# Kernel optimization log

Hardware: AMD Instinct MI355X
Metric: run time of the kernel (lower is better)

Reference implementation:

```python
import jax, jax.numpy as jnp
import numpy as np

N = 50000       # nodes
E = 800000      # edges (avg degree 16)
IN_DIM = 128
EDGE_DIM = 32
OUT_DIM = 128


def setup_inputs() -> dict:
    key = jax.random.key(0)
    ks = jax.random.split(key, 7)
    nfeat = jax.random.normal(ks[0], (N, IN_DIM), jnp.float32)
    etype = jax.random.normal(ks[1], (E, EDGE_DIM), jnp.float32)
    src = jax.random.randint(ks[2], (E,), 0, N)
    dst = jax.random.randint(ks[3], (E,), 0, N)
    scaled = lambda k, shape, fan: jax.random.normal(k, shape, jnp.float32) / np.sqrt(fan).astype(np.float32)
    W_edge = scaled(ks[4], (OUT_DIM, EDGE_DIM), EDGE_DIM)          # edge_map.weight
    W_ne = scaled(ks[5], (OUT_DIM, IN_DIM + OUT_DIM), IN_DIM + OUT_DIM)  # fc_neigh_edge.weight
    b_ne = jnp.zeros((OUT_DIM,), jnp.float32)
    W_self = scaled(ks[6], (OUT_DIM, IN_DIM), IN_DIM)              # fc_self.weight
    b_self = jnp.zeros((OUT_DIM,), jnp.float32)
    eps = jnp.zeros((1,), jnp.float32)                             # init_eps = 0, not learned
    return dict(nfeat=nfeat, etype=etype, src=src, dst=dst,
                W_edge=W_edge, W_ne=W_ne, b_ne=b_ne,
                W_self=W_self, b_self=b_self, eps=eps)


def reference(nfeat, etype, src, dst, W_edge, W_ne, b_ne, W_self, b_self, eps):
    # per-edge message: relu(fc_neigh_edge(cat(src_h, edge_map(etype))))
    # split W_ne to avoid materializing the concatenated [E, in+out] tensor
    W1 = W_ne[:, :IN_DIM]    # acts on src node features
    W2 = W_ne[:, IN_DIM:]    # acts on mapped edge features
    eh = etype @ W_edge.T                              # [E, out]
    src_h = nfeat[src]                                 # gather [E, in]
    m = jax.nn.relu(src_h @ W1.T + eh @ W2.T + b_ne)   # [E, out]
    # max-reduce messages to destination nodes (DGL max reducer; 0 for isolated nodes)
    neigh = jax.ops.segment_max(m, dst, num_segments=N)
    deg = jax.ops.segment_sum(jnp.ones((E,), m.dtype), dst, num_segments=N)
    neigh = jnp.where((deg > 0)[:, None], neigh, jnp.zeros((), m.dtype))
    out = (1.0 + eps) * neigh + (nfeat @ W_self.T + b_self)
    return out
```

## Files before the change

### kernel.cpp

```cpp
#include <hip/hip_runtime.h>
#include <hip/hip_bf16.h>

#define NNODES 50000
#define NEDGES 800000
#define IN_DIM 128
#define EDGE_DIM 32
#define OUT_DIM 128
#define KDIM 160
#define A_STRIDE 168
#define NS 136
#define MT_STRIDE 72
#define NT (NEDGES / 64)
#define EG 1024
#define NSCB 49

typedef __attribute__((ext_vector_type(8))) short short8;
typedef __attribute__((ext_vector_type(4))) short short4v;
typedef __attribute__((ext_vector_type(4))) float floatx4;

__device__ __forceinline__ short f2bf(float f) {
    union { float f; unsigned u; } v; v.f = f;
    unsigned r = (v.u + 0x7FFFu + ((v.u >> 16) & 1u)) >> 16;
    return (short)r;
}

__device__ __forceinline__ void store_bf4(short* p, floatx4 v) {
    short4v s;
    s.x = f2bf(v.x); s.y = f2bf(v.y); s.z = f2bf(v.z); s.w = f2bf(v.w);
    *(short4v*)p = s;
}

__device__ __forceinline__ void store_bf8(short* p, floatx4 a, floatx4 b) {
    short8 s;
    s[0] = f2bf(a.x); s[1] = f2bf(a.y); s[2] = f2bf(a.z); s[3] = f2bf(a.w);
    s[4] = f2bf(b.x); s[5] = f2bf(b.y); s[6] = f2bf(b.z); s[7] = f2bf(b.w);
    *(short8*)p = s;
}

#define MFMA8(ACC, A0, A1, B0, B1, B2, B3)                                        \
    ACC[0][0] = __builtin_amdgcn_mfma_f32_16x16x32_bf16(A0, B0, ACC[0][0], 0, 0, 0); \
    ACC[0][1] = __builtin_amdgcn_mfma_f32_16x16x32_bf16(A0, B1, ACC[0][1], 0, 0, 0); \
    ACC[0][2] = __builtin_amdgcn_mfma_f32_16x16x32_bf16(A0, B2, ACC[0][2], 0, 0, 0); \
    ACC[0][3] = __builtin_amdgcn_mfma_f32_16x16x32_bf16(A0, B3, ACC[0][3], 0, 0, 0); \
    ACC[1][0] = __builtin_amdgcn_mfma_f32_16x16x32_bf16(A1, B0, ACC[1][0], 0, 0, 0); \
    ACC[1][1] = __builtin_amdgcn_mfma_f32_16x16x32_bf16(A1, B1, ACC[1][1], 0, 0, 0); \
    ACC[1][2] = __builtin_amdgcn_mfma_f32_16x16x32_bf16(A1, B2, ACC[1][2], 0, 0, 0); \
    ACC[1][3] = __builtin_amdgcn_mfma_f32_16x16x32_bf16(A1, B3, ACC[1][3], 0, 0, 0);

__global__ __launch_bounds__(256) void prep_kernel(
    const float* __restrict__ nfeat, const int* __restrict__ dst,
    const float* __restrict__ W_edge, const float* __restrict__ W_ne,
    const float* __restrict__ W_self,
    int* __restrict__ cnt, short* __restrict__ nfB,
    short* __restrict__ WcatB, short* __restrict__ WselfB)
{
    int gid = blockIdx.x * 256 + threadIdx.x;
    int GS = gridDim.x * 256;
    for (int i = gid; i < NNODES * IN_DIM / 8; i += GS) {
        floatx4 a = ((const floatx4*)nfeat)[2 * i];
        floatx4 b = ((const floatx4*)nfeat)[2 * i + 1];
        store_bf8(nfB + 8 * i, a, b);
    }
    for (int idx = gid; idx < OUT_DIM * KDIM + OUT_DIM * IN_DIM; idx += GS) {
        if (idx < OUT_DIM * KDIM) {
            int n = idx / KDIM, k = idx - n * KDIM;
            float val;
            if (k < IN_DIM) {
                val = W_ne[n * 256 + k];
            } else {
                int j = k - IN_DIM;
                float s = 0.f;
                for (int kk = 0; kk < 128; ++kk)
                    s += W_ne[n * 256 + 128 + kk] * W_edge[kk * 32 + j];
                val = s;
            }
            WcatB[idx] = f2bf(val);
        } else {
            int s = idx - OUT_DIM * KDIM;
            WselfB[s] = f2bf(W_self[s]);
        }
    }
    for (int e = gid; e < NEDGES; e += GS)
        atomicAdd(&cnt[dst[e]], 1);
}

__global__ __launch_bounds__(256) void scan_part(const int* __restrict__ cnt,
                                                 int* __restrict__ bsum) {
    __shared__ int red[256];
    int b = blockIdx.x, t = threadIdx.x;
    int idx = b * 1024 + t * 4;
    int4 v = {0, 0, 0, 0};
    if (idx < NNODES) v = *(const int4*)(cnt + idx);
    red[t] = v.x + v.y + v.z + v.w;
    __syncthreads();
    for (int off = 128; off > 0; off >>= 1) {
        if (t < off) red[t] += red[t + off];
        __syncthreads();
    }
    if (t == 0) bsum[b] = red[0];
}

__global__ __launch_bounds__(64) void scan_mid(const int* __restrict__ bsum,
                                               int* __restrict__ boff) {
    __shared__ int a[64], b[64];
    int t = threadIdx.x;
    int v = (t < NSCB) ? bsum[t] : 0;
    a[t] = v;
    __syncthreads();
    int* in = a; int* out = b;
    for (int off = 1; off < 64; off <<= 1) {
        out[t] = in[t] + (t >= off ? in[t - off] : 0);
        __syncthreads();
        int* tmp = in; in = out; out = tmp;
    }
    if (t < NSCB) boff[t] = in[t] - v;
}

__global__ __launch_bounds__(256) void scan_write(const int* __restrict__ cnt,
                                                  const int* __restrict__ boff,
                                                  int* __restrict__ cur) {
    __shared__ int a[256], bb[256];
    int b = blockIdx.x, t = threadIdx.x;
    int idx = b * 1024 + t * 4;
    int4 v = {0, 0, 0, 0};
    if (idx < NNODES) v = *(const int4*)(cnt + idx);
    int s = v.x + v.y + v.z + v.w;
    a[t] = s;
    __syncthreads();
    int* in = a; int* out = bb;
    for (int off = 1; off < 256; off <<= 1) {
        out[t] = in[t] + (t >= off ? in[t - off] : 0);
        __syncthreads();
        int* tmp = in; in = out; out = tmp;
    }
    if (idx < NNODES) {
        int base = boff[b] + in[t] - s;
        cur[idx] = base;     base += v.x;
        cur[idx + 1] = base; base += v.y;
        cur[idx + 2] = base; base += v.z;
        cur[idx + 3] = base;
    }
}

__global__ __launch_bounds__(256) void scatter_kernel(
    const int* __restrict__ src, const int* __restrict__ dst,
    const float* __restrict__ etype,
    int* __restrict__ cur,
    int* __restrict__ esd, short* __restrict__ escT) {
    const int tid = threadIdx.x;
    const int lane = tid & 63;
    const int g = lane & 7;
    const int ldr = lane & ~7;
    const int grp = tid >> 3;
    const int GS = gridDim.x * 32;
    for (int e = blockIdx.x * 32 + grp; e < NEDGES; e += GS) {
        int pos = 0;
        if (g == 0) {
            int d = dst[e];
            int s = src[e];
            pos = atomicAdd(&cur[d], 1);
            esd[pos] = (int)((unsigned)s | ((unsigned)d << 16));
        }
        pos = __shfl(pos, ldr);
        floatx4 v = ((const floatx4*)(etype + (size_t)e * 32))[g];
        store_bf4(escT + (size_t)pos * 32 + g * 4, v);
    }
}

__global__ __launch_bounds__(256, 4) void edge_kernel(
    const short* __restrict__ nfB, const short* __restrict__ escT,
    const int* __restrict__ esd, const float* __restrict__ b_ne,
    const short* __restrict__ WcatB, float* __restrict__ out)
{
    __shared__ short As[64 * A_STRIDE];
    __shared__ unsigned short mT[128 * MT_STRIDE];
    __shared__ short dstL[2][64];

    const int tid = threadIdx.x;
    const int lane = tid & 63;
    const int w = tid >> 6;
    const int li = lane & 15, q = lane >> 4;

    short8 bf[2][5];
    #pragma unroll
    for (int ct = 0; ct < 2; ++ct)
        #pragma unroll
        for (int kk = 0; kk < 5; ++kk)
            bf[ct][kk] = *(const short8*)(WcatB +
                (size_t)(w * 32 + ct * 16 + li) * KDIM + kk * 32 + q * 8);

    float bias[2];
    #pragma unroll
    for (int ct = 0; ct < 2; ++ct) bias[ct] = b_ne[w * 32 + ct * 16 + li];

    const int ee = tid >> 2, ec = tid & 3;

    short8 pv0, pv1, pv2, pv3;
    short8 pe;
    int rsd = 0;
    int psd = 0;

    const int tA = blockIdx.x;

    {
        int sd = esd[tA * 64 + ee];
        int s = sd & 0xFFFF;
        const short8* nr = (const short8*)(nfB + (size_t)s * 128);
        pv0 = nr[4 * ec]; pv1 = nr[4 * ec + 1];
        pv2 = nr[4 * ec + 2]; pv3 = nr[4 * ec + 3];
        pe = *(const short8*)(escT + (size_t)(tA * 64 + ee) * 32 + ec * 8);

        int tB = tA + EG;
        int sdB = 0;
        if (tB < NT) sdB = esd[tB * 64 + ee];

        short* ap = As + ee * A_STRIDE + 32 * ec;
        *(short8*)(ap)      = pv0;
        *(short8*)(ap + 8)  = pv1;
        *(short8*)(ap + 16) = pv2;
        *(short8*)(ap + 24) = pv3;
        *(short8*)(As + ee * A_STRIDE + IN_DIM + 8 * ec) = pe;
        if (ec == 0) dstL[0][ee] = (short)((unsigned)sd >> 16);

        if (tB < NT) {
            int sB = sdB & 0xFFFF;
            const short8* nrB = (const short8*)(nfB + (size_t)sB * 128);
            pv0 = nrB[4 * ec]; pv1 = nrB[4 * ec + 1];
            pv2 = nrB[4 * ec + 2]; pv3 = nrB[4 * ec + 3];
            pe = *(const short8*)(escT + (size_t)(tB * 64 + ee) * 32 + ec * 8);
            rsd = sdB;
            int tC = tB + EG;
            if (tC < NT) psd = esd[tC * 64 + ee];
        }
    }

    int it = 0;
    for (int t = tA; t < NT; t += EG, ++it) {
        const int cb = it & 1, nb = cb ^ 1;

        asm volatile("s_waitcnt lgkmcnt(0)" ::: "memory");
        __builtin_amdgcn_s_barrier();

        floatx4 acc[4][2];
        #pragma unroll
        for (int i = 0; i < 4; ++i)
            #pragma unroll
            for (int j = 0; j < 2; ++j)
                acc[i][j] = (floatx4){0.f, 0.f, 0.f, 0.f};

        __builtin_amdgcn_s_setprio(1);
        #pragma unroll
        for (int kk = 0; kk < 5; ++kk) {
            short8 a0 = *(const short8*)(As + (0 * 16 + li) * A_STRIDE + kk * 32 + q * 8);
            short8 a1 = *(const short8*)(As + (1 * 16 + li) * A_STRIDE + kk * 32 + q * 8);
            short8 a2 = *(const short8*)(As + (2 * 16 + li) * A_STRIDE + kk * 32 + q * 8);
            short8 a3 = *(const short8*)(As + (3 * 16 + li) * A_STRIDE + kk * 32 + q * 8);
            acc[0][0] = __builtin_amdgcn_mfma_f32_16x16x32_bf16(a0, bf[0][kk], acc[0][0], 0, 0, 0);
            acc[0][1] = __builtin_amdgcn_mfma_f32_16x16x32_bf16(a0, bf[1][kk], acc[0][1], 0, 0, 0);
            acc[1][0] = __builtin_amdgcn_mfma_f32_16x16x32_bf16(a1, bf[0][kk], acc[1][0], 0, 0, 0);
            acc[1][1] = __builtin_amdgcn_mfma_f32_16x16x32_bf16(a1, bf[1][kk], acc[1][1], 0, 0, 0);
            acc[2][0] = __builtin_amdgcn_mfma_f32_16x16x32_bf16(a2, bf[0][kk], acc[2][0], 0, 0, 0);
            acc[2][1] = __builtin_amdgcn_mfma_f32_16x16x32_bf16(a2, bf[1][kk], acc[2][1], 0, 0, 0);
            acc[3][0] = __builtin_amdgcn_mfma_f32_16x16x32_bf16(a3, bf[0][kk], acc[3][0], 0, 0, 0);
            acc[3][1] = __builtin_amdgcn_mfma_f32_16x16x32_bf16(a3, bf[1][kk], acc[3][1], 0, 0, 0);
        }
        __builtin_amdgcn_s_setprio(0);

        #pragma unroll
        for (int rt = 0; rt < 4; ++rt) {
            #pragma unroll
            for (int ct = 0; ct < 2; ++ct) {
                floatx4 a = acc[rt][ct];
                short4v s;
                float v0 = a.x + bias[ct]; s.x = f2bf(v0 > 0.f ? v0 : 0.f);
                float v1 = a.y + bias[ct]; s.y = f2bf(v1 > 0.f ? v1 : 0.f);
                float v2 = a.z + bias[ct]; s.z = f2bf(v2 > 0.f ? v2 : 0.f);
                float v3 = a.w + bias[ct]; s.w = f2bf(v3 > 0.f ? v3 : 0.f);
                *(short4v*)((short*)mT + (w * 32 + ct * 16 + li) * MT_STRIDE
                            + rt * 16 + q * 4) = s;
            }
        }
        asm volatile("s_waitcnt lgkmcnt(0)" ::: "memory");
        __builtin_amdgcn_s_barrier();

        {
            int tn = t + EG;
            if (tn < NT) {
                short* ap = As + ee * A_STRIDE + 32 * ec;
                *(short8*)(ap)      = pv0;
                *(short8*)(ap + 8)  = pv1;
                *(short8*)(ap + 16) = pv2;
                *(short8*)(ap + 24) = pv3;
                *(short8*)(As + ee * A_STRIDE + IN_DIM + 8 * ec) = pe;
                if (ec == 0) dstL[nb][ee] = (short)((unsigned)rsd >> 16);

                int sd2 = psd;
                int t2 = tn + EG;
                if (t2 < NT) {
                    int t3 = t2 + EG;
                    if (t3 < NT) psd = esd[t3 * 64 + ee];
                    int s2 = sd2 & 0xFFFF;
                    const short8* nr2 = (const short8*)(nfB + (size_t)s2 * 128);
                    pv0 = nr2[4 * ec]; pv1 = nr2[4 * ec + 1];
                    pv2 = nr2[4 * ec + 2]; pv3 = nr2[4 * ec + 3];
                    pe = *(const short8*)(escT + (size_t)(t2 * 64 + ee) * 32 + ec * 8);
                    rsd = sd2;
                }
            }
        }
        __builtin_amdgcn_sched_barrier(0);

        {
            int c = tid & 127, h = tid >> 7;
            int r0 = h * 32;
            unsigned mval[32];
            #pragma unroll
            for (int j = 0; j < 4; ++j) {
                short8 v = *(const short8*)((const short*)mT + c * MT_STRIDE
                                            + r0 + 8 * j);
                #pragma unroll
                for (int k = 0; k < 8; ++k)
                    mval[8 * j + k] = (unsigned short)v[k];
            }
            const short8* dls = (const short8*)(&dstL[cb][r0]);
            int curd = 0;
            unsigned best = 0;
            #pragma unroll
            for (int j = 0; j < 4; ++j) {
                short8 dv = dls[j];
                #pragma unroll
                for (int k = 0; k < 8; ++k) {
                    int r = 8 * j + k;
                    int d = __builtin_amdgcn_readfirstlane(
                        (int)(unsigned short)dv[k]);
                    if (r == 0) {
                        curd = d; best = mval[0];
                    } else if (d != curd) {
                        atomicMax((int*)out + (size_t)curd * 128 + c,
                                  (int)(best << 16));
                        curd = d; best = mval[r];
                    } else {
                        best = best > mval[r] ? best : mval[r];
                    }
                }
            }
            atomicMax((int*)out + (size_t)curd * 128 + c, (int)(best << 16));
        }
    }
}

__global__ __launch_bounds__(256) void node_kernel(
    const short* __restrict__ nfB, const float* __restrict__ b_self,
    const float* __restrict__ eps, const short* __restrict__ WselfB,
    float* __restrict__ out)
{
    __shared__ short As[64 * NS];
    __shared__ short Bs[128 * NS];
    const int tid = threadIdx.x;
    const int n0 = blockIdx.x * 64;

    {
        int r = tid >> 1, h = tid & 1;
        const short8* g = (const short8*)(WselfB + r * 128 + h * 64);
        short* l = Bs + r * NS + h * 64;
        #pragma unroll
        for (int c = 0; c < 8; ++c)
            *(short8*)(l + 8 * c) = g[c];
    }
    {
        int r = tid >> 2, c = tid & 3;
        int n = n0 + r;
        short* ap = As + r * NS + 32 * c;
        if (n < NNODES) {
            const short8* nr = (const short8*)(nfB + (size_t)n * 128);
            #pragma unroll
            for (int j = 0; j < 4; ++j)
                *(short8*)(ap + 8 * j) = nr[4 * c + j];
        } else {
            #pragma unroll
            for (int j = 0; j < 4; ++j)
                *(short8*)(ap + 8 * j) = (short8){0,0,0,0,0,0,0,0};
        }
    }
    __syncthreads();

    const int lane = tid & 63;
    const int w = tid >> 6;
    const int et = w & 1;
    const int nh = w >> 1;
    const int li = lane & 15, q = lane >> 4;

    floatx4 acc[2][4];
    #pragma unroll
    for (int i = 0; i < 2; ++i)
        #pragma unroll
        for (int j = 0; j < 4; ++j)
            acc[i][j] = (floatx4){0.f, 0.f, 0.f, 0.f};

    const short* Ab = As + (et * 32 + li) * NS + q * 8;
    const short* Bb = Bs + (nh * 64 + li) * NS + q * 8;
    #pragma unroll
    for (int kk = 0; kk < 4; ++kk) {
        short8 a0 = *(const short8*)(Ab + kk * 32);
        short8 a1 = *(const short8*)(Ab + 16 * NS + kk * 32);
        short8 b0 = *(const short8*)(Bb + kk * 32);
        short8 b1 = *(const short8*)(Bb + 16 * NS + kk * 32);
        short8 b2 = *(const short8*)(Bb + 32 * NS + kk * 32);
        short8 b3 = *(const short8*)(Bb + 48 * NS + kk * 32);
        MFMA8(acc, a0, a1, b0, b1, b2, b3)
    }

    const float epsv = 1.0f + eps[0];
    #pragma unroll
    for (int ta = 0; ta < 2; ++ta) {
        #pragma unroll
        for (int r = 0; r < 4; ++r) {
            int n = n0 + et * 32 + ta * 16 + q * 4 + r;
            if (n < NNODES) {
                #pragma unroll
                for (int tb = 0; tb < 4; ++tb) {
                    int o = nh * 64 + tb * 16 + li;
                    float v = acc[ta][tb][r] + b_self[o]
                            + epsv * out[(size_t)n * 128 + o];
                    out[(size_t)n * 128 + o] = v;
                }
            }
        }
    }
}

__global__ void prep_w(const float* __restrict__ W_edge,
                       const float* __restrict__ W_ne,
                       const float* __restrict__ W_self,
                       short* __restrict__ WcatB, short* __restrict__ WselfB)
{
    int idx = blockIdx.x * 256 + threadIdx.x;
    if (idx < OUT_DIM * KDIM) {
        int n = idx / KDIM, k = idx - n * KDIM;
        float val;
        if (k < IN_DIM) {
            val = W_ne[n * 256 + k];
        } else {
            int j = k - IN_DIM;
            float s = 0.f;
            for (int kk = 0; kk < 128; ++kk)
                s += W_ne[n * 256 + 128 + kk] * W_edge[kk * 32 + j];
            val = s;
        }
        WcatB[idx] = f2bf(val);
    } else if (idx < OUT_DIM * KDIM + OUT_DIM * IN_DIM) {
        int s = idx - OUT_DIM * KDIM;
        WselfB[s] = f2bf(W_self[s]);
    }
}

__global__ __launch_bounds__(256) void edge_direct(
    const float* __restrict__ nfeat, const float* __restrict__ etype,
    const int* __restrict__ src, const int* __restrict__ dst,
    const float* __restrict__ b_ne, const short* __restrict__ WcatB,
    float* __restrict__ out)
{
    __shared__ short As[64 * A_STRIDE];
    __shared__ short Bs[128 * A_STRIDE];
    const int tid = threadIdx.x;
    const int e0 = blockIdx.x * 64;
    {
        int r = tid >> 1, h = tid & 1;
        const short8* g = (const short8*)(WcatB + r * KDIM + h * 80);
        short* l = Bs + r * A_STRIDE + h * 80;
        #pragma unroll
        for (int c = 0; c < 10; ++c) *(short8*)(l + 8 * c) = g[c];
    }
    {
        const floatx4* ge = (const floatx4*)(etype + (size_t)e0 * 32);
        #pragma unroll
        for (int i = 0; i < 2; ++i) {
            int f = tid + i * 256;
            int e = f >> 3, c = f & 7;
            store_bf4(As + e * A_STRIDE + IN_DIM + 4 * c, ge[f]);
        }
    }
    {
        int g = tid & 15, eo = tid >> 4;
        #pragma unroll
        for (int p = 0; p < 4; ++p) {
            int e = eo + p * 16;
            int s = src[e0 + e];
            const floatx4* row = (const floatx4*)(nfeat + (size_t)s * 128);
            floatx4 v0 = row[g];
            floatx4 v1 = row[g + 16];
            store_bf4(As + e * A_STRIDE + 4 * g, v0);
            store_bf4(As + e * A_STRIDE + 64 + 4 * g, v1);
        }
    }
    __syncthreads();
    const int lane = tid & 63;
    const int w = tid >> 6;
    const int et = w & 1, nh = w >> 1;
    const int li = lane & 15, q = lane >> 4;
    floatx4 acc[2][4];
    #pragma unroll
    for (int i = 0; i < 2; ++i)
        #pragma unroll
        for (int j = 0; j < 4; ++j)
            acc[i][j] = (floatx4){0.f, 0.f, 0.f, 0.f};
    const short* Ab = As + (et * 32 + li) * A_STRIDE + q * 8;
    const short* Bb = Bs + (nh * 64 + li) * A_STRIDE + q * 8;
    #pragma unroll
    for (int kk = 0; kk < 5; ++kk) {
        short8 a0 = *(const short8*)(Ab + kk * 32);
        short8 a1 = *(const short8*)(Ab + 16 * A_STRIDE + kk * 32);
        short8 b0 = *(const short8*)(Bb + kk * 32);
        short8 b1 = *(const short8*)(Bb + 16 * A_STRIDE + kk * 32);
        short8 b2 = *(const short8*)(Bb + 32 * A_STRIDE + kk * 32);
        short8 b3 = *(const short8*)(Bb + 48 * A_STRIDE + kk * 32);
        MFMA8(acc, a0, a1, b0, b1, b2, b3)
    }
    #pragma unroll
    for (int ta = 0; ta < 2; ++ta) {
        #pragma unroll
        for (int r = 0; r < 4; ++r) {
            int el = et * 32 + ta * 16 + q * 4 + r;
            int d = dst[e0 + el];
            int* nrow = (int*)out + (size_t)d * 128;
            #pragma unroll
            for (int tb = 0; tb < 4; ++tb) {
                int o = nh * 64 + tb * 16 + li;
                float v = acc[ta][tb][r] + b_ne[o];
                v = v > 0.f ? v : 0.f;
                atomicMax(nrow + o, __float_as_int(v));
            }
        }
    }
}

__global__ __launch_bounds__(256) void node_direct(
    const float* __restrict__ nfeat, const float* __restrict__ b_self,
    const float* __restrict__ eps, const short* __restrict__ WselfB,
    float* __restrict__ out)
{
    __shared__ short As[64 * NS];
    __shared__ short Bs[128 * NS];
    const int tid = threadIdx.x;
    const int n0 = blockIdx.x * 64;
    {
        int r = tid >> 1, h = tid & 1;
        const short8* g = (const short8*)(WselfB + r * 128 + h * 64);
        short* l = Bs + r * NS + h * 64;
        #pragma unroll
        for (int c = 0; c < 8; ++c) *(short8*)(l + 8 * c) = g[c];
    }
    {
        int r = tid >> 2, fi = tid & 3;
        int n = n0 + r;
        if (n < NNODES) {
            const floatx4* row = (const floatx4*)(nfeat + (size_t)n * 128);
            #pragma unroll
            for (int p = 0; p < 8; ++p) {
                int f = fi + 4 * p;
                store_bf4(As + r * NS + 4 * f, row[f]);
            }
        } else {
            #pragma unroll
            for (int p = 0; p < 8; ++p) {
                int f = fi + 4 * p;
                *(short4v*)(As + r * NS + 4 * f) = (short4v){0, 0, 0, 0};
            }
        }
    }
    __syncthreads();
    const int lane = tid & 63;
    const int w = tid >> 6;
    const int et = w & 1, nh = w >> 1;
    const int li = lane & 15, q = lane >> 4;
    floatx4 acc[2][4];
    #pragma unroll
    for (int i = 0; i < 2; ++i)
        #pragma unroll
        for (int j = 0; j < 4; ++j)
            acc[i][j] = (floatx4){0.f, 0.f, 0.f, 0.f};
    const short* Ab = As + (et * 32 + li) * NS + q * 8;
    const short* Bb = Bs + (nh * 64 + li) * NS + q * 8;
    #pragma unroll
    for (int kk = 0; kk < 4; ++kk) {
        short8 a0 = *(const short8*)(Ab + kk * 32);
        short8 a1 = *(const short8*)(Ab + 16 * NS + kk * 32);
        short8 b0 = *(const short8*)(Bb + kk * 32);
        short8 b1 = *(const short8*)(Bb + 16 * NS + kk * 32);
        short8 b2 = *(const short8*)(Bb + 32 * NS + kk * 32);
        short8 b3 = *(const short8*)(Bb + 48 * NS + kk * 32);
        MFMA8(acc, a0, a1, b0, b1, b2, b3)
    }
    const float epsv = 1.0f + eps[0];
    #pragma unroll
    for (int ta = 0; ta < 2; ++ta) {
        #pragma unroll
        for (int r = 0; r < 4; ++r) {
            int n = n0 + et * 32 + ta * 16 + q * 4 + r;
            if (n < NNODES) {
                #pragma unroll
                for (int tb = 0; tb < 4; ++tb) {
                    int o = nh * 64 + tb * 16 + li;
                    float v = acc[ta][tb][r] + b_self[o]
                            + epsv * out[(size_t)n * 128 + o];
                    out[(size_t)n * 128 + o] = v;
                }
            }
        }
    }
}

extern "C" void kernel_launch(void* const* d_in, const int* in_sizes, int n_in,
                              void* d_out, int out_size, void* d_ws, size_t ws_size,
                              hipStream_t stream) {
    const float* nfeat  = (const float*)d_in[0];
    const float* etype  = (const float*)d_in[1];
    const int*   src    = (const int*)d_in[2];
    const int*   dst    = (const int*)d_in[3];
    const float* W_edge = (const float*)d_in[4];
    const float* W_ne   = (const float*)d_in[5];
    const float* b_ne   = (const float*)d_in[6];
    const float* W_self = (const float*)d_in[7];
    const float* b_self = (const float*)d_in[8];
    const float* eps    = (const float*)d_in[9];
    float* out = (float*)d_out;

    char* ws = (char*)d_ws;
    size_t off = 0;
    auto alloc = [&](size_t bytes) { void* p = ws + off; off = (off + bytes + 255) & ~(size_t)255; return p; };
    int*   cnt    = (int*)alloc((size_t)NNODES * 4);
    int*   cur    = (int*)alloc((size_t)NNODES * 4);
    int*   esd    = (int*)alloc((size_t)NEDGES * 4);
    short* escT   = (short*)alloc((size_t)NEDGES * EDGE_DIM * 2);
    short* nfB    = (short*)alloc((size_t)NNODES * IN_DIM * 2);
    short* WcatB  = (short*)alloc((size_t)OUT_DIM * KDIM * 2);
    short* WselfB = (short*)alloc((size_t)OUT_DIM * IN_DIM * 2);
    int*   bsum   = (int*)alloc((size_t)NSCB * 4);
    int*   boff   = (int*)alloc((size_t)NSCB * 4);
    size_t need = off;

    if (ws_size >= need) {
        hipMemsetAsync(cnt, 0, (size_t)NNODES * 4, stream);
        hipMemsetAsync(out, 0, (size_t)NNODES * OUT_DIM * sizeof(float), stream);
        prep_kernel<<<1024, 256, 0, stream>>>(nfeat, dst, W_edge, W_ne, W_self,
                                              cnt, nfB, WcatB, WselfB);
        scan_part<<<NSCB, 256, 0, stream>>>(cnt, bsum);
        scan_mid<<<1, 64, 0, stream>>>(bsum, boff);
        scan_write<<<NSCB, 256, 0, stream>>>(cnt, boff, cur);
        scatter_kernel<<<2048, 256, 0, stream>>>(src, dst, etype, cur, esd, escT);
        edge_kernel<<<EG, 256, 0, stream>>>(nfB, escT, esd, b_ne, WcatB, out);
        node_kernel<<<(NNODES + 63) / 64, 256, 0, stream>>>(nfB, b_self, eps,
                                                            WselfB, out);
    } else {
        short* WcatB2  = (short*)d_ws;
        short* WselfB2 = WcatB2 + (size_t)OUT_DIM * KDIM;
        hipMemsetAsync(out, 0, (size_t)NNODES * 128 * sizeof(float), stream);
        prep_w<<<144, 256, 0, stream>>>(W_edge, W_ne, W_self, WcatB2, WselfB2);
        edge_direct<<<NEDGES / 64, 256, 0, stream>>>(nfeat, etype, src, dst,
                                                     b_ne, WcatB2, out);
        node_direct<<<(NNODES + 63) / 64, 256, 0, stream>>>(nfeat, b_self, eps,
                                                            WselfB2, out);
    }
}
```

Before: 345.9 us.

## Split edge scatter into index-only scatter and sorted-order etype gather

The combined scatter kernel, which atomically placed each edge and wrote its bf16 edge features to a scattered position, is replaced by two kernels. The first uses one thread per edge to do the atomic placement and records the original edge id alongside the packed src/dst. The second walks the sorted positions, gathers etype rows by original id and writes escT contiguously. The aim is coalesced writes and denser atomics, at the cost of an extra launch, an 8-byte epack array, and the edge kernel reading 8-byte records to get the 4-byte src/dst field.

```diff
diff --git a/kernel.cpp b/kernel.cpp
--- a/kernel.cpp
+++ b/kernel.cpp
@@ -142,34 +142,40 @@
     }
 }
 
-__global__ __launch_bounds__(256) void scatter_kernel(
-    const int* __restrict__ src, const int* __restrict__ dst,
-    const float* __restrict__ etype,
-    int* __restrict__ cur,
-    int* __restrict__ esd, short* __restrict__ escT) {
+__global__ void scatter_lite(const int* __restrict__ src,
+                             const int* __restrict__ dst,
+                             int* __restrict__ cur,
+                             int2* __restrict__ epack) {
+    int e = blockIdx.x * 256 + threadIdx.x;
+    if (e < NEDGES) {
+        int d = dst[e];
+        int s = src[e];
+        int pos = atomicAdd(&cur[d], 1);
+        int2 r;
+        r.x = (int)((unsigned)s | ((unsigned)d << 16));
+        r.y = e;
+        epack[pos] = r;
+    }
+}
+
+__global__ __launch_bounds__(256) void gather_conv(
+    const int2* __restrict__ epack, const float* __restrict__ etype,
+    short* __restrict__ escT) {
     const int tid = threadIdx.x;
     const int lane = tid & 63;
     const int g = lane & 7;
-    const int ldr = lane & ~7;
     const int grp = tid >> 3;
     const int GS = gridDim.x * 32;
-    for (int e = blockIdx.x * 32 + grp; e < NEDGES; e += GS) {
-        int pos = 0;
-        if (g == 0) {
-            int d = dst[e];
-            int s = src[e];
-            pos = atomicAdd(&cur[d], 1);
-            esd[pos] = (int)((unsigned)s | ((unsigned)d << 16));
-        }
-        pos = __shfl(pos, ldr);
+    for (int p = blockIdx.x * 32 + grp; p < NEDGES; p += GS) {
+        int e = epack[p].y;
         floatx4 v = ((const floatx4*)(etype + (size_t)e * 32))[g];
-        store_bf4(escT + (size_t)pos * 32 + g * 4, v);
+        store_bf4(escT + (size_t)p * 32 + g * 4, v);
     }
 }
 
 __global__ __launch_bounds__(256, 4) void edge_kernel(
     const short* __restrict__ nfB, const short* __restrict__ escT,
-    const int* __restrict__ esd, const float* __restrict__ b_ne,
+    const int2* __restrict__ epack, const float* __restrict__ b_ne,
     const short* __restrict__ WcatB, float* __restrict__ out)
 {
     __shared__ short As[64 * A_STRIDE];
@@ -203,7 +209,7 @@
     const int tA = blockIdx.x;
 
     {
-        int sd = esd[tA * 64 + ee];
+        int sd = epack[tA * 64 + ee].x;
         int s = sd & 0xFFFF;
         const short8* nr = (const short8*)(nfB + (size_t)s * 128);
         pv0 = nr[4 * ec]; pv1 = nr[4 * ec + 1];
@@ -212,7 +218,7 @@
 
         int tB = tA + EG;
         int sdB = 0;
-        if (tB < NT) sdB = esd[tB * 64 + ee];
+        if (tB < NT) sdB = epack[tB * 64 + ee].x;
 
         short* ap = As + ee * A_STRIDE + 32 * ec;
         *(short8*)(ap)      = pv0;
@@ -230,7 +236,7 @@
             pe = *(const short8*)(escT + (size_t)(tB * 64 + ee) * 32 + ec * 8);
             rsd = sdB;
             int tC = tB + EG;
-            if (tC < NT) psd = esd[tC * 64 + ee];
+            if (tC < NT) psd = epack[tC * 64 + ee].x;
         }
     }
 
@@ -298,7 +304,7 @@
                 int t2 = tn + EG;
                 if (t2 < NT) {
                     int t3 = t2 + EG;
-                    if (t3 < NT) psd = esd[t3 * 64 + ee];
+                    if (t3 < NT) psd = epack[t3 * 64 + ee].x;
                     int s2 = sd2 & 0xFFFF;
                     const short8* nr2 = (const short8*)(nfB + (size_t)s2 * 128);
                     pv0 = nr2[4 * ec]; pv1 = nr2[4 * ec + 1];
@@ -630,7 +636,7 @@
     auto alloc = [&](size_t bytes) { void* p = ws + off; off = (off + bytes + 255) & ~(size_t)255; return p; };
     int*   cnt    = (int*)alloc((size_t)NNODES * 4);
     int*   cur    = (int*)alloc((size_t)NNODES * 4);
-    int*   esd    = (int*)alloc((size_t)NEDGES * 4);
+    int2*  epack  = (int2*)alloc((size_t)NEDGES * 8);
     short* escT   = (short*)alloc((size_t)NEDGES * EDGE_DIM * 2);
     short* nfB    = (short*)alloc((size_t)NNODES * IN_DIM * 2);
     short* WcatB  = (short*)alloc((size_t)OUT_DIM * KDIM * 2);
@@ -647,8 +653,10 @@
         scan_part<<<NSCB, 256, 0, stream>>>(cnt, bsum);
         scan_mid<<<1, 64, 0, stream>>>(bsum, boff);
         scan_write<<<NSCB, 256, 0, stream>>>(cnt, boff, cur);
-        scatter_kernel<<<2048, 256, 0, stream>>>(src, dst, etype, cur, esd, escT);
-        edge_kernel<<<EG, 256, 0, stream>>>(nfB, escT, esd, b_ne, WcatB, out);
+        scatter_lite<<<(NEDGES + 255) / 256, 256, 0, stream>>>(
+            src, dst, cur, epack);
+        gather_conv<<<2048, 256, 0, stream>>>(epack, etype, escT);
+        edge_kernel<<<EG, 256, 0, stream>>>(nfB, escT, epack, b_ne, WcatB, out);
         node_kernel<<<(NNODES + 63) / 64, 256, 0, stream>>>(nfB, b_self, eps,
                                                             WselfB, out);
     } else {
```

After: 387.3 us. 1.12x slower.
